# Kernel optimization log

Hardware: AMD Instinct MI355X
Metric: run time of the kernel (lower is better)

The kernel has to match this reference:

```python
import jax, jax.numpy as jnp
import numpy as np

NUM_HEADS = 16
NUM_KV_HEADS = 4
HEAD_SIZE = 128
SCALE = 1.0 / np.sqrt(128.0).astype(np.float32)
NEG_INF = -1e30


def setup_inputs() -> dict:
    key = jax.random.key(0)
    kq, kk, kv = jax.random.split(key, 3)
    B, S = 2, 2048
    query = jax.random.normal(kq, (B, NUM_HEADS, S, HEAD_SIZE), dtype=jnp.float32)
    k = jax.random.normal(kk, (B, NUM_KV_HEADS, S, HEAD_SIZE), dtype=jnp.float32)
    v = jax.random.normal(kv, (B, NUM_KV_HEADS, S, HEAD_SIZE), dtype=jnp.float32)
    return {"query": query, "key": k, "value": v}


def _attn(query, key, value):
    # query: [B, H, S, D]; key/value: [B, Hkv, S, D]; GQA with group = H // Hkv
    B, H, S, D = query.shape
    Hkv = key.shape[1]
    G = H // Hkv
    q = query.reshape(B, Hkv, G, S, D)
    # scores: [B, Hkv, G, Sq, Sk]
    scores = jnp.einsum('bkgsd,bktd->bkgst', q, key) * jnp.float32(SCALE)
    causal = jnp.tril(jnp.ones((S, S), dtype=bool))  # [Sq, Sk]
    scores = jnp.where(causal, scores, jnp.float32(NEG_INF))
    probs = jax.nn.softmax(scores, axis=-1)
    out = jnp.einsum('bkgst,bktd->bkgsd', probs, value)  # [B, Hkv, G, S, D]
    out = out.reshape(B, H, S, D)
    # transpose(1,2).reshape -> [B, S, H*D]
    return out.transpose(0, 2, 1, 3).reshape(B, S, H * D)


def reference(query, key, value):
    return _attn(query, key, value)
```

## Files before the change

### kernel.cpp

```cpp
#include <hip/hip_runtime.h>


#define S_LEN 2048
#define DH    128
#define NH    16
#define NKVH  4
#define NB    2
#define TQ    128
#define TK    64
#define NQT   (S_LEN / TQ)
#define QSCALE 0.12752749610559243f

typedef __attribute__((ext_vector_type(8))) short short8;
typedef __attribute__((ext_vector_type(4))) float f32x4;

#if __has_builtin(__builtin_amdgcn_exp2f)
#define EX2(x) __builtin_amdgcn_exp2f(x)
#else
#define EX2(x) exp2f(x)
#endif

__device__ __forceinline__ unsigned pk2(float a, float b) {
    union { float f; unsigned u; } x, y; x.f = a; y.f = b;
    return ((x.u + 0x8000u) >> 16) | ((y.u + 0x8000u) & 0xffff0000u);
}
__device__ __forceinline__ void cp16(const void* g, void* lds) {
    __builtin_amdgcn_global_load_lds(
        (const __attribute__((address_space(1))) void*)g,
        (__attribute__((address_space(3))) void*)lds, 16, 0, 0);
}

__global__ __launch_bounds__(256, 4)
void prepack(const float* __restrict__ K, const float* __restrict__ V,
             unsigned short* __restrict__ Kb, unsigned short* __restrict__ Vt) {
    if (blockIdx.y == 0) {
        const long long flat = (long long)blockIdx.x * 2048 + threadIdx.x * 8;
        const int s = (int)(flat >> 7) & (S_LEN - 1);
        const int d0 = (int)flat & 127;
        const float* p = K + flat;
        float4 x = *(const float4*)p;
        float4 y = *(const float4*)(p + 4);
        const int cs = (d0 >> 3) ^ (s & 7);
        uint4 o;
        o.x = pk2(x.x, x.y); o.y = pk2(x.z, x.w);
        o.z = pk2(y.x, y.y); o.w = pk2(y.z, y.w);
        *(uint4*)(Kb + (flat & ~127LL) + cs * 8) = o;
    } else {
        const int x = blockIdx.x;
        const int bkvh = x >> 7, sblk = (x >> 2) & 31, q = x & 3;
        const int tid = threadIdx.x;
        __shared__ unsigned Lt[64][17];
        const float* base = V + (size_t)bkvh * S_LEN * DH + (size_t)sblk * 64 * DH + q * 32;
#pragma unroll
        for (int j = 0; j < 2; ++j) {
            const int e = tid + j * 256;
            const int s = e >> 3, c4 = e & 7;
            float4 v = *(const float4*)(base + (size_t)s * DH + c4 * 4);
            Lt[s][c4 * 2]     = pk2(v.x, v.y);
            Lt[s][c4 * 2 + 1] = pk2(v.z, v.w);
        }
        __syncthreads();
        const unsigned short* lt = (const unsigned short*)&Lt[0][0];
        const int d_loc = tid >> 3, pc = tid & 7;
        const int d = q * 32 + d_loc;
        const int c_log = pc ^ (d & 7);
        unsigned short vv[8];
#pragma unroll
        for (int j = 0; j < 8; ++j) {
            const int kp = c_log * 8 + j;
            const int kv = (kp & 3) * 16 + (kp >> 2);
            vv[j] = lt[kv * 34 + d_loc];
        }
        uint4 o;
        o.x = (unsigned)vv[0] | ((unsigned)vv[1] << 16);
        o.y = (unsigned)vv[2] | ((unsigned)vv[3] << 16);
        o.z = (unsigned)vv[4] | ((unsigned)vv[5] << 16);
        o.w = (unsigned)vv[6] | ((unsigned)vv[7] << 16);
        *(uint4*)(Vt + (size_t)bkvh * S_LEN * DH + (size_t)d * S_LEN + sblk * 64 + pc * 8) = o;
    }
}

__global__ __launch_bounds__(256, 2)
void attn_fwd(const float* __restrict__ Q,
              const unsigned short* __restrict__ Kb,
              const unsigned short* __restrict__ Vtg,
              float* __restrict__ O) {
    const int n   = blockIdx.x;
    const int g   = n & 7;
    const int b   = g >> 2;
    const int kvh = g & 3;
    const int kk  = n >> 3;
    const int h   = kvh * 4 + (kk & 3);
    const int x   = kk >> 2;
    const int qt  = (x & 8) ? (x & 7) : (15 - (x & 7));

    const int tid  = threadIdx.x;
    const int w    = tid >> 6;
    const int lane = tid & 63;
    const int quad = lane >> 4;
    const int l16  = lane & 15;
    const int swz  = l16 & 7;

    __shared__ alignas(16) unsigned short Kl[2][TK][DH];
    __shared__ alignas(16) unsigned short Vl[2][DH][TK];
    __shared__ alignas(16) unsigned short Pl[TQ][64];

    const unsigned short* kb = Kb  + ((size_t)b * NKVH + kvh) * (size_t)(S_LEN * DH);
    const unsigned short* vb = Vtg + ((size_t)b * NKVH + kvh) * (size_t)(S_LEN * DH);

    const int nt  = 2 * qt + 2;
    const int ntw = 2 * qt + 1 + (w >> 1);

    auto stage = [&](int nb, int tt) {
        const char* ks = (const char*)(kb + (size_t)tt * TK * DH);
        char* kd = (char*)&Kl[nb][0][0] + w * 4096;
#pragma unroll
        for (int i = 0; i < 4; ++i)
            cp16(ks + w * 4096 + i * 1024 + lane * 16, kd + i * 1024);
        const char* vs = (const char*)vb + (size_t)tt * (TK * 2);
        char* vd = (char*)&Vl[nb][0][0] + w * 4096;
#pragma unroll
        for (int i = 0; i < 4; ++i) {
            const int row = w * 32 + i * 8 + (lane >> 3);
            cp16(vs + (size_t)row * (S_LEN * 2) + (lane & 7) * 16, vd + i * 1024);
        }
    };

    stage(0, 0);

    const int wq0 = qt * TQ + w * 32;
    short8 aq[2][4];
#pragma unroll
    for (int sub = 0; sub < 2; ++sub) {
        const float* qp = Q + (((size_t)b * NH + h) * S_LEN + wq0 + sub * 16 + l16) * DH;
#pragma unroll
        for (int dc = 0; dc < 4; ++dc) {
            float4 xx = *(const float4*)(qp + dc * 32 + quad * 8);
            float4 yy = *(const float4*)(qp + dc * 32 + quad * 8 + 4);
            union { unsigned u[4]; short8 s; } tq;
            tq.u[0] = pk2(xx.x * QSCALE, xx.y * QSCALE);
            tq.u[1] = pk2(xx.z * QSCALE, xx.w * QSCALE);
            tq.u[2] = pk2(yy.x * QSCALE, yy.y * QSCALE);
            tq.u[3] = pk2(yy.z * QSCALE, yy.w * QSCALE);
            aq[sub][dc] = tq.s;
        }
    }

    f32x4 o[2][8];
#pragma unroll
    for (int sub = 0; sub < 2; ++sub)
#pragma unroll
        for (int ch = 0; ch < 8; ++ch) o[sub][ch] = (f32x4){0.f, 0.f, 0.f, 0.f};
    float lsum[2][4];
#pragma unroll
    for (int sub = 0; sub < 2; ++sub)
#pragma unroll
        for (int r = 0; r < 4; ++r) lsum[sub][r] = 0.f;

    __syncthreads();

    int cur = 0;
    for (int t = 0; t < nt; ++t) {
        if (t + 1 < nt) stage(cur ^ 1, t + 1);
        if (t < ntw) {
            const int j0 = t * TK;
            const bool diag = (t == ntw - 1);
            f32x4 s[2][4];
#pragma unroll
            for (int sub = 0; sub < 2; ++sub)
#pragma unroll
                for (int k4 = 0; k4 < 4; ++k4) s[sub][k4] = (f32x4){0.f, 0.f, 0.f, 0.f};
#pragma unroll
            for (int dc = 0; dc < 4; ++dc) {
#pragma unroll
                for (int k4 = 0; k4 < 4; ++k4) {
                    short8 bk = *(const short8*)&Kl[cur][k4 * 16 + l16][((dc * 4 + quad) ^ swz) * 8];
                    s[0][k4] = __builtin_amdgcn_mfma_f32_16x16x32_bf16(aq[0][dc], bk, s[0][k4], 0, 0, 0);
                    s[1][k4] = __builtin_amdgcn_mfma_f32_16x16x32_bf16(aq[1][dc], bk, s[1][k4], 0, 0, 0);
                }
            }
#pragma unroll
            for (int sub = 0; sub < 2; ++sub) {
                const int rb = wq0 + sub * 16 + quad * 4;
#pragma unroll
                for (int r = 0; r < 4; ++r) {
                    float v0 = s[sub][0][r], v1 = s[sub][1][r];
                    float v2 = s[sub][2][r], v3 = s[sub][3][r];
                    if (diag) {
                        const int row = rb + r;
                        if (j0 + l16      > row) v0 = -1e30f;
                        if (j0 + 16 + l16 > row) v1 = -1e30f;
                        if (j0 + 32 + l16 > row) v2 = -1e30f;
                        if (j0 + 48 + l16 > row) v3 = -1e30f;
                    }
                    float p0 = EX2(v0), p1 = EX2(v1), p2 = EX2(v2), p3 = EX2(v3);
                    lsum[sub][r] += (p0 + p1) + (p2 + p3);
                    const int prow = w * 32 + sub * 16 + quad * 4 + r;
                    const int wcol = (l16 * 8) ^ ((prow & 7) << 4);
                    *(uint2*)((char*)&Pl[0][0] + prow * 128 + wcol) =
                        make_uint2(pk2(p0, p1), pk2(p2, p3));
                }
            }
            const int rx = (l16 & 7) << 4;
#pragma unroll
            for (int kc = 0; kc < 2; ++kc) {
                const int cb = kc * 64 + quad * 16;
                short8 ap0 = *(const short8*)((const char*)&Pl[0][0] + (w * 32 + l16) * 128 + (cb ^ rx));
                short8 ap1 = *(const short8*)((const char*)&Pl[0][0] + (w * 32 + 16 + l16) * 128 + (cb ^ rx));
#pragma unroll
                for (int ch = 0; ch < 8; ++ch) {
                    short8 bv = *(const short8*)&Vl[cur][ch * 16 + l16][((kc * 4 + quad) ^ swz) * 8];
                    o[0][ch] = __builtin_amdgcn_mfma_f32_16x16x32_bf16(ap0, bv, o[0][ch], 0, 0, 0);
                    o[1][ch] = __builtin_amdgcn_mfma_f32_16x16x32_bf16(ap1, bv, o[1][ch], 0, 0, 0);
                }
            }
        }
        __syncthreads();
        cur ^= 1;
    }

#pragma unroll
    for (int sub = 0; sub < 2; ++sub) {
#pragma unroll
        for (int r = 0; r < 4; ++r) {
            float rs = lsum[sub][r];
            rs += __shfl_xor(rs, 1);
            rs += __shfl_xor(rs, 2);
            rs += __shfl_xor(rs, 4);
            rs += __shfl_xor(rs, 8);
            const float invl = 1.f / rs;
            const int row = wq0 + sub * 16 + quad * 4 + r;
            float* op = O + ((size_t)b * S_LEN + row) * (NH * DH) + h * DH;
#pragma unroll
            for (int ch = 0; ch < 8; ++ch)
                op[ch * 16 + l16] = o[sub][ch][r] * invl;
        }
    }
}

extern "C" void kernel_launch(void* const* d_in, const int* in_sizes, int n_in,
                              void* d_out, int out_size, void* d_ws, size_t ws_size,
                              hipStream_t stream) {
    const float* Q = (const float*)d_in[0];
    const float* K = (const float*)d_in[1];
    const float* V = (const float*)d_in[2];
    float* O = (float*)d_out;
    unsigned short* Kb = (unsigned short*)d_ws;
    unsigned short* Vt = Kb + (size_t)NB * NKVH * S_LEN * DH;
    dim3 pgrid(NB * NKVH * (S_LEN / 16), 2);
    prepack<<<pgrid, 256, 0, stream>>>(K, V, Kb, Vt);
    attn_fwd<<<dim3(512), 256, 0, stream>>>(Q, Kb, Vt, O);
}
```

Before: 158.1 us.

## Balance causal work by pairing query tiles and splitting long tiles across blocks

Each block now processes exactly 17 key tiles. Role-0 blocks handle a short query tile fully and then start the long tile's first part. Role-1 blocks process the remaining key tiles of the long tile and write unnormalized partials plus row sums to workspace. A new combine kernel merges the two partials and normalizes in the output. The aim is to remove the load imbalance of the causal triangle, at the cost of an extra kernel launch and extra global traffic for the partials.

```diff
diff --git a/kernel.cpp b/kernel.cpp
--- a/kernel.cpp
+++ b/kernel.cpp
@@ -84,15 +84,19 @@
 void attn_fwd(const float* __restrict__ Q,
               const unsigned short* __restrict__ Kb,
               const unsigned short* __restrict__ Vtg,
-              float* __restrict__ O) {
-    const int n   = blockIdx.x;
-    const int g   = n & 7;
-    const int b   = g >> 2;
-    const int kvh = g & 3;
-    const int kk  = n >> 3;
-    const int h   = kvh * 4 + (kk & 3);
-    const int x   = kk >> 2;
-    const int qt  = (x & 8) ? (x & 7) : (15 - (x & 7));
+              float* __restrict__ O,
+              float* __restrict__ Opart,
+              float* __restrict__ Lpart) {
+    const int n    = blockIdx.x;
+    const int g    = n & 7;
+    const int b    = g >> 2;
+    const int kvh  = g & 3;
+    const int kk   = n >> 3;
+    const int h    = kvh * 4 + (kk & 3);
+    const int pr   = kk >> 2;
+    const int a    = pr & 7;
+    const int role = pr >> 3;
+    const int sid  = ((b * NH + h) << 3) + a;
 
     const int tid  = threadIdx.x;
     const int w    = tid >> 6;
@@ -101,6 +105,12 @@
     const int l16  = lane & 15;
     const int swz  = l16 & 7;
 
+    int qt0, kt00, nr0, qt1; bool two_seg;
+    if (role == 0) { qt0 = a;      kt00 = 0;         nr0 = 2 * a + 2;
+                     qt1 = 15 - a; two_seg = true; }
+    else           { qt0 = 15 - a; kt00 = 15 - 2*a;  nr0 = 17;
+                     qt1 = 0;      two_seg = false; }
+
     __shared__ alignas(16) unsigned short Kl[2][TK][DH];
     __shared__ alignas(16) unsigned short Vl[2][DH][TK];
     __shared__ alignas(16) unsigned short Pl[TQ][64];
@@ -108,63 +118,67 @@
     const unsigned short* kb = Kb  + ((size_t)b * NKVH + kvh) * (size_t)(S_LEN * DH);
     const unsigned short* vb = Vtg + ((size_t)b * NKVH + kvh) * (size_t)(S_LEN * DH);
 
-    const int nt  = 2 * qt + 2;
-    const int ntw = 2 * qt + 1 + (w >> 1);
-
-    auto stage = [&](int nb, int tt) {
-        const char* ks = (const char*)(kb + (size_t)tt * TK * DH);
-        char* kd = (char*)&Kl[nb][0][0] + w * 4096;
+    auto stage = [&](int nb_, int kt) {
+        const char* ks = (const char*)(kb + (size_t)kt * TK * DH);
+        char* kd = (char*)&Kl[nb_][0][0] + w * 4096;
 #pragma unroll
         for (int i = 0; i < 4; ++i)
             cp16(ks + w * 4096 + i * 1024 + lane * 16, kd + i * 1024);
-        const char* vs = (const char*)vb + (size_t)tt * (TK * 2);
-        char* vd = (char*)&Vl[nb][0][0] + w * 4096;
+        const char* vs = (const char*)vb + (size_t)kt * (TK * 2);
+        char* vd = (char*)&Vl[nb_][0][0] + w * 4096;
 #pragma unroll
         for (int i = 0; i < 4; ++i) {
             const int row = w * 32 + i * 8 + (lane >> 3);
             cp16(vs + (size_t)row * (S_LEN * 2) + (lane & 7) * 16, vd + i * 1024);
         }
     };
-
-    stage(0, 0);
-
-    const int wq0 = qt * TQ + w * 32;
+    auto ktof = [&](int r) { return r < nr0 ? kt00 + r : r - nr0; };
+
+    stage(0, ktof(0));
+
+    int qt  = qt0;
+    int wq0 = qt * TQ + w * 32;
+    int ntw = 2 * qt + 1 + (w >> 1);
+
     short8 aq[2][4];
+    auto loadQ = [&]() {
+#pragma unroll
+        for (int sub = 0; sub < 2; ++sub) {
+            const float* qp = Q + (((size_t)b * NH + h) * S_LEN + wq0 + sub * 16 + l16) * DH;
+#pragma unroll
+            for (int dc = 0; dc < 4; ++dc) {
+                float4 xx = *(const float4*)(qp + dc * 32 + quad * 8);
+                float4 yy = *(const float4*)(qp + dc * 32 + quad * 8 + 4);
+                union { unsigned u[4]; short8 s; } tq;
+                tq.u[0] = pk2(xx.x * QSCALE, xx.y * QSCALE);
+                tq.u[1] = pk2(xx.z * QSCALE, xx.w * QSCALE);
+                tq.u[2] = pk2(yy.x * QSCALE, yy.y * QSCALE);
+                tq.u[3] = pk2(yy.z * QSCALE, yy.w * QSCALE);
+                aq[sub][dc] = tq.s;
+            }
+        }
+    };
+    loadQ();
+
+    f32x4 o[2][8];
+    float lsum[2][4];
 #pragma unroll
     for (int sub = 0; sub < 2; ++sub) {
-        const float* qp = Q + (((size_t)b * NH + h) * S_LEN + wq0 + sub * 16 + l16) * DH;
-#pragma unroll
-        for (int dc = 0; dc < 4; ++dc) {
-            float4 xx = *(const float4*)(qp + dc * 32 + quad * 8);
-            float4 yy = *(const float4*)(qp + dc * 32 + quad * 8 + 4);
-            union { unsigned u[4]; short8 s; } tq;
-            tq.u[0] = pk2(xx.x * QSCALE, xx.y * QSCALE);
-            tq.u[1] = pk2(xx.z * QSCALE, xx.w * QSCALE);
-            tq.u[2] = pk2(yy.x * QSCALE, yy.y * QSCALE);
-            tq.u[3] = pk2(yy.z * QSCALE, yy.w * QSCALE);
-            aq[sub][dc] = tq.s;
-        }
-    }
-
-    f32x4 o[2][8];
-#pragma unroll
-    for (int sub = 0; sub < 2; ++sub)
 #pragma unroll
         for (int ch = 0; ch < 8; ++ch) o[sub][ch] = (f32x4){0.f, 0.f, 0.f, 0.f};
-    float lsum[2][4];
-#pragma unroll
-    for (int sub = 0; sub < 2; ++sub)
 #pragma unroll
         for (int r = 0; r < 4; ++r) lsum[sub][r] = 0.f;
+    }
 
     __syncthreads();
 
     int cur = 0;
-    for (int t = 0; t < nt; ++t) {
-        if (t + 1 < nt) stage(cur ^ 1, t + 1);
-        if (t < ntw) {
-            const int j0 = t * TK;
-            const bool diag = (t == ntw - 1);
+    for (int r = 0; r < 17; ++r) {
+        if (r + 1 < 17) stage(cur ^ 1, ktof(r + 1));
+        const int kt = ktof(r);
+        if (kt < ntw) {
+            const int j0 = kt * TK;
+            const bool diag = (kt == ntw - 1);
             f32x4 s[2][4];
 #pragma unroll
             for (int sub = 0; sub < 2; ++sub)
@@ -183,19 +197,19 @@
             for (int sub = 0; sub < 2; ++sub) {
                 const int rb = wq0 + sub * 16 + quad * 4;
 #pragma unroll
-                for (int r = 0; r < 4; ++r) {
-                    float v0 = s[sub][0][r], v1 = s[sub][1][r];
-                    float v2 = s[sub][2][r], v3 = s[sub][3][r];
+                for (int rr = 0; rr < 4; ++rr) {
+                    float v0 = s[sub][0][rr], v1 = s[sub][1][rr];
+                    float v2 = s[sub][2][rr], v3 = s[sub][3][rr];
                     if (diag) {
-                        const int row = rb + r;
+                        const int row = rb + rr;
                         if (j0 + l16      > row) v0 = -1e30f;
                         if (j0 + 16 + l16 > row) v1 = -1e30f;
                         if (j0 + 32 + l16 > row) v2 = -1e30f;
                         if (j0 + 48 + l16 > row) v3 = -1e30f;
                     }
                     float p0 = EX2(v0), p1 = EX2(v1), p2 = EX2(v2), p3 = EX2(v3);
-                    lsum[sub][r] += (p0 + p1) + (p2 + p3);
-                    const int prow = w * 32 + sub * 16 + quad * 4 + r;
+                    lsum[sub][rr] += (p0 + p1) + (p2 + p3);
+                    const int prow = w * 32 + sub * 16 + quad * 4 + rr;
                     const int wcol = (l16 * 8) ^ ((prow & 7) << 4);
                     *(uint2*)((char*)&Pl[0][0] + prow * 128 + wcol) =
                         make_uint2(pk2(p0, p1), pk2(p2, p3));
@@ -217,24 +231,88 @@
         }
         __syncthreads();
         cur ^= 1;
-    }
-
+        if (two_seg && r == nr0 - 1) {
+#pragma unroll
+            for (int sub = 0; sub < 2; ++sub) {
+#pragma unroll
+                for (int rr = 0; rr < 4; ++rr) {
+                    float rs = lsum[sub][rr];
+                    rs += __shfl_xor(rs, 1);
+                    rs += __shfl_xor(rs, 2);
+                    rs += __shfl_xor(rs, 4);
+                    rs += __shfl_xor(rs, 8);
+                    const float invl = 1.f / rs;
+                    const int row = wq0 + sub * 16 + quad * 4 + rr;
+                    float* op = O + ((size_t)b * S_LEN + row) * (NH * DH) + h * DH;
+#pragma unroll
+                    for (int ch = 0; ch < 8; ++ch)
+                        op[ch * 16 + l16] = o[sub][ch][rr] * invl;
+                }
+            }
+            qt = qt1; wq0 = qt * TQ + w * 32; ntw = 2 * qt + 1 + (w >> 1);
+            loadQ();
+#pragma unroll
+            for (int sub = 0; sub < 2; ++sub) {
+#pragma unroll
+                for (int ch = 0; ch < 8; ++ch) o[sub][ch] = (f32x4){0.f, 0.f, 0.f, 0.f};
+#pragma unroll
+                for (int rr = 0; rr < 4; ++rr) lsum[sub][rr] = 0.f;
+            }
+        }
+    }
+
+    float* lb = Lpart + (size_t)(role * 256 + sid) * 128;
 #pragma unroll
     for (int sub = 0; sub < 2; ++sub) {
 #pragma unroll
-        for (int r = 0; r < 4; ++r) {
-            float rs = lsum[sub][r];
+        for (int rr = 0; rr < 4; ++rr) {
+            float rs = lsum[sub][rr];
             rs += __shfl_xor(rs, 1);
             rs += __shfl_xor(rs, 2);
             rs += __shfl_xor(rs, 4);
             rs += __shfl_xor(rs, 8);
-            const float invl = 1.f / rs;
-            const int row = wq0 + sub * 16 + quad * 4 + r;
-            float* op = O + ((size_t)b * S_LEN + row) * (NH * DH) + h * DH;
+            const int rl = w * 32 + sub * 16 + quad * 4 + rr;
+            if (l16 == 0) lb[rl] = rs;
+            float* op;
+            if (role == 0) {
+                const int row = wq0 + sub * 16 + quad * 4 + rr;
+                op = O + ((size_t)b * S_LEN + row) * (NH * DH) + h * DH;
+            } else {
+                op = Opart + (size_t)sid * (128 * 128) + (size_t)rl * 128;
+            }
 #pragma unroll
             for (int ch = 0; ch < 8; ++ch)
-                op[ch * 16 + l16] = o[sub][ch][r] * invl;
-        }
+                op[ch * 16 + l16] = o[sub][ch][rr];
+        }
+    }
+}
+
+__global__ __launch_bounds__(256)
+void combine(const float* __restrict__ Opart, const float* __restrict__ Lpart,
+             float* __restrict__ O) {
+    const int blk = blockIdx.x;
+    const int sid = blk >> 2;
+    const int qp  = blk & 3;
+    const int bh = sid >> 3, a = sid & 7;
+    const int b = bh >> 4, h = bh & 15;
+    const int qt = 15 - a;
+    const float* o1 = Opart + (size_t)sid * (128 * 128);
+    const float* l0 = Lpart + (size_t)sid * 128;
+    const float* l1 = Lpart + (size_t)(256 + sid) * 128;
+    const int tid = threadIdx.x;
+#pragma unroll
+    for (int i = 0; i < 4; ++i) {
+        const int idx = qp * 1024 + i * 256 + tid;
+        const int row = idx >> 5;
+        const int c4  = idx & 31;
+        const float inv = 1.f / (l0[row] + l1[row]);
+        float* op = O + ((size_t)b * S_LEN + qt * 128 + row) * (NH * DH) + h * DH + c4 * 4;
+        const float4 x = *(const float4*)op;
+        const float4 y = ((const float4*)o1)[idx];
+        float4 z;
+        z.x = (x.x + y.x) * inv; z.y = (x.y + y.y) * inv;
+        z.z = (x.z + y.z) * inv; z.w = (x.w + y.w) * inv;
+        *(float4*)op = z;
     }
 }
 
@@ -247,7 +325,10 @@
     float* O = (float*)d_out;
     unsigned short* Kb = (unsigned short*)d_ws;
     unsigned short* Vt = Kb + (size_t)NB * NKVH * S_LEN * DH;
+    float* Opart = (float*)(Vt + (size_t)NB * NKVH * S_LEN * DH);
+    float* Lpart = Opart + (size_t)256 * 128 * 128;
     dim3 pgrid(NB * NKVH * (S_LEN / 16), 2);
     prepack<<<pgrid, 256, 0, stream>>>(K, V, Kb, Vt);
-    attn_fwd<<<dim3(512), 256, 0, stream>>>(Q, Kb, Vt, O);
-}
+    attn_fwd<<<dim3(512), 256, 0, stream>>>(Q, Kb, Vt, O, Opart, Lpart);
+    combine<<<dim3(1024), 256, 0, stream>>>(Opart, Lpart, O);
+}
```

New measurement: 149.6 us. 5.3% less time.
